# Kernel tuning notes

Hardware: AMD Instinct MI355X
Metric: run time of the kernel (lower is better)

The kernel has to match this reference:

```python
import jax, jax.numpy as jnp
import numpy as np

B, CIN, H, W = 16, 256, 56, 56
D, HEADS, KS, PAD, STRIDE, M = 256, 8, 3, 1, 1, 4
K = KS * KS
N = D // HEADS
# relative_indices: sum of window coords, flattened row-major, values in [0, 2*KS-2]
REL = (np.arange(KS)[:, None] + np.arange(KS)[None, :]).reshape(-1)


def setup_inputs() -> dict:
    key = jax.random.key(0)
    ks = jax.random.split(key, 7)
    return {
        "x": jax.random.normal(ks[0], (B, CIN, H, W), jnp.float32),
        "q": jax.random.normal(ks[1], (B, D, 1), jnp.float32),
        "Wk": jax.random.normal(ks[2], (D, CIN), jnp.float32) * 0.05,
        "Wv": jax.random.normal(ks[3], (D, CIN), jnp.float32) * 0.05,
        "pos_emb": jax.random.normal(ks[4], (1, 2 * KS - 1), jnp.float32),
        "Wlin": jax.random.normal(ks[5], (1, M), jnp.float32),
        "Wproj": jax.random.normal(ks[6], (D, D), jnp.float32) * 0.05,
    }


def _unfold(t):
    # torch nn.Unfold: (B,C,H,W) -> (B, C*K, L); patches feature dim ordered (C, kh, kw)
    p = jax.lax.conv_general_dilated_patches(
        t, (KS, KS), (STRIDE, STRIDE), [(PAD, PAD), (PAD, PAD)])
    b, _, ho, wo = p.shape
    return p.reshape(b, -1, ho * wo), ho, wo


def reference(x, q, Wk, Wv, pos_emb, Wlin, Wproj):
    b = x.shape[0]
    k = jnp.einsum('oc,bchw->bohw', Wk, x)  # 1x1 conv, no bias
    v = jnp.einsum('oc,bchw->bohw', Wv, x)
    ku, ho, wo = _unfold(k)
    vu, _, _ = _unfold(v)
    L = ho * wo
    ku = ku.reshape(b, HEADS, N, K, L)  # (b, h, n, k, l)
    vu = vu.reshape(b, HEADS, N, K, L)
    qh = q.reshape(b, HEADS, N)  # learned per-batch query, d=1 squeezed
    attn = jnp.einsum('bhn,bhnkl->bhlk', qh, ku)  # (b,h,l,K)
    attn = attn + pos_emb[0, REL]  # relative position bias, shape (K,)
    attn = jax.nn.softmax(attn, axis=-1)
    # repeat d(=1) -> m identical rows then Linear(m,1,no bias): equals scale by sum(Wlin)
    attn = attn * jnp.sum(Wlin)
    out = jnp.einsum('bhlk,bhnkl->bhnl', attn, vu)  # (b,h,n,l)
    out = out.reshape(b, D, ho, wo)  # fold with kernel 1 == reshape
    return jnp.einsum('oc,bchw->bohw', Wproj, out)  # 1x1 proj conv
```

## Files before the change

### kernel.cpp

```cpp
#include <hip/hip_runtime.h>

#define B_     16
#define D_     256
#define HEADS_ 8
#define N_     32
#define H_     56
#define W_     56
#define L_     3136
#define LDA    40

typedef short short8 __attribute__((ext_vector_type(8)));
typedef float f32x4  __attribute__((ext_vector_type(4)));

__device__ __forceinline__ unsigned short f2bf(float f) {
    union { float f; unsigned u; } c; c.f = f;
    unsigned u = c.u;
    u += 0x7fffu + ((u >> 16) & 1u);
    return (unsigned short)(u >> 16);
}

__global__ __launch_bounds__(256) void transpose_x_kernel(
    const float* __restrict__ x, unsigned short* __restrict__ Xt)
{
    __shared__ float tile[64][65];
    const int bb = blockIdx.z;
    const int c0 = blockIdx.y * 64;
    const int l0 = blockIdx.x * 64;
    const int t  = threadIdx.x;
    const int g4 = (t & 15) * 4;
    const int rr = t >> 4;

    const float* xb = x + ((size_t)bb * D_ + c0) * L_ + l0;
#pragma unroll
    for (int i = 0; i < 4; ++i) {
        const int c = rr + i * 16;
        float4 v = *(const float4*)(xb + (size_t)c * L_ + g4);
        *(float4*)&tile[c][g4] = v;
    }
    __syncthreads();
    unsigned short* Xb = Xt + ((size_t)bb * L_ + l0) * D_ + c0;
#pragma unroll
    for (int i = 0; i < 4; ++i) {
        const int l = rr + i * 16;
        uint2 o;
        o.x = (unsigned)f2bf(tile[g4 + 0][l]) | ((unsigned)f2bf(tile[g4 + 1][l]) << 16);
        o.y = (unsigned)f2bf(tile[g4 + 2][l]) | ((unsigned)f2bf(tile[g4 + 3][l]) << 16);
        *(uint2*)(Xb + (size_t)l * D_ + g4) = o;
    }
}

__global__ __launch_bounds__(256) void convert_w_kernel(
    const float* __restrict__ w0, const float* __restrict__ w1,
    const float* __restrict__ w2, unsigned short* __restrict__ o0,
    unsigned short* __restrict__ o1, unsigned short* __restrict__ o2)
{
    const float* src; unsigned short* dst;
    if (blockIdx.y == 0)      { src = w0; dst = o0; }
    else if (blockIdx.y == 1) { src = w1; dst = o1; }
    else                      { src = w2; dst = o2; }
    const int i = (blockIdx.x * 256 + threadIdx.x) * 4;
    float4 v = *(const float4*)(src + i);
    uint2 o;
    o.x = (unsigned)f2bf(v.x) | ((unsigned)f2bf(v.y) << 16);
    o.y = (unsigned)f2bf(v.z) | ((unsigned)f2bf(v.w) << 16);
    *(uint2*)(dst + i) = o;
}

__global__ __launch_bounds__(256) void gemm_kv_mfma(
    const unsigned short* __restrict__ Xt, const unsigned short* __restrict__ Wkb,
    const unsigned short* __restrict__ Wvb, const float* __restrict__ q,
    unsigned short* __restrict__ Vo, float* __restrict__ S)
{
    __shared__ unsigned short Aks[128][LDA];
    __shared__ unsigned short Avs[128][LDA];
    __shared__ unsigned short Bs[64][LDA];

    const int bb = blockIdx.z;
    const int d0 = blockIdx.y * 128;
    const int l0 = blockIdx.x * 64;
    const int t  = threadIdx.x;
    const int w    = t >> 6;
    const int lane = t & 63;
    const int col  = lane & 15;
    const int quad = lane >> 4;

    f32x4 accK[2][4], accV[2][4];
#pragma unroll
    for (int mi = 0; mi < 2; ++mi)
#pragma unroll
        for (int ni = 0; ni < 4; ++ni) {
            accK[mi][ni] = (f32x4){0.f, 0.f, 0.f, 0.f};
            accV[mi][ni] = (f32x4){0.f, 0.f, 0.f, 0.f};
        }

    const int srow = t >> 2;
    const int skc  = (t & 3) * 8;
    const unsigned short* Xrow = Xt + ((size_t)bb * L_ + l0 + srow) * D_ + skc;
    const unsigned short* Wk0  = Wkb + (size_t)(d0 + srow) * D_ + skc;
    const unsigned short* Wk1  = Wkb + (size_t)(d0 + 64 + srow) * D_ + skc;
    const unsigned short* Wv0  = Wvb + (size_t)(d0 + srow) * D_ + skc;
    const unsigned short* Wv1  = Wvb + (size_t)(d0 + 64 + srow) * D_ + skc;

    for (int kt = 0; kt < 8; ++kt) {
        const int c0 = kt * 32;
        uint4 xg  = *(const uint4*)(Xrow + c0);
        uint4 kg0 = *(const uint4*)(Wk0 + c0);
        uint4 kg1 = *(const uint4*)(Wk1 + c0);
        uint4 vg0 = *(const uint4*)(Wv0 + c0);
        uint4 vg1 = *(const uint4*)(Wv1 + c0);

        __syncthreads();
        *(uint4*)&Bs[srow][skc]        = xg;
        *(uint4*)&Aks[srow][skc]       = kg0;
        *(uint4*)&Aks[srow + 64][skc]  = kg1;
        *(uint4*)&Avs[srow][skc]       = vg0;
        *(uint4*)&Avs[srow + 64][skc]  = vg1;
        __syncthreads();

        short8 ak0 = *(const short8*)&Aks[w * 32 + col][quad * 8];
        short8 ak1 = *(const short8*)&Aks[w * 32 + 16 + col][quad * 8];
        short8 av0 = *(const short8*)&Avs[w * 32 + col][quad * 8];
        short8 av1 = *(const short8*)&Avs[w * 32 + 16 + col][quad * 8];
        short8 bfr[4];
#pragma unroll
        for (int ni = 0; ni < 4; ++ni)
            bfr[ni] = *(const short8*)&Bs[ni * 16 + col][quad * 8];

#pragma unroll
        for (int ni = 0; ni < 4; ++ni) {
            accK[0][ni] = __builtin_amdgcn_mfma_f32_16x16x32_bf16(ak0, bfr[ni], accK[0][ni], 0, 0, 0);
            accK[1][ni] = __builtin_amdgcn_mfma_f32_16x16x32_bf16(ak1, bfr[ni], accK[1][ni], 0, 0, 0);
            accV[0][ni] = __builtin_amdgcn_mfma_f32_16x16x32_bf16(av0, bfr[ni], accV[0][ni], 0, 0, 0);
            accV[1][ni] = __builtin_amdgcn_mfma_f32_16x16x32_bf16(av1, bfr[ni], accV[1][ni], 0, 0, 0);
        }
    }

#pragma unroll
    for (int mi = 0; mi < 2; ++mi)
#pragma unroll
        for (int ni = 0; ni < 4; ++ni)
#pragma unroll
            for (int r = 0; r < 4; ++r) {
                const int d = d0 + w * 32 + mi * 16 + quad * 4 + r;
                const int l = l0 + ni * 16 + col;
                Vo[((size_t)bb * D_ + d) * L_ + l] = f2bf(accV[mi][ni][r]);
            }

    const int hh = blockIdx.y * 4 + w;
    float qv[2][4];
#pragma unroll
    for (int mi = 0; mi < 2; ++mi)
#pragma unroll
        for (int r = 0; r < 4; ++r)
            qv[mi][r] = q[bb * D_ + hh * N_ + mi * 16 + quad * 4 + r];

#pragma unroll
    for (int ni = 0; ni < 4; ++ni) {
        float s = 0.f;
#pragma unroll
        for (int mi = 0; mi < 2; ++mi)
#pragma unroll
            for (int r = 0; r < 4; ++r)
                s = fmaf(qv[mi][r], accK[mi][ni][r], s);
        s += __shfl_xor(s, 16, 64);
        s += __shfl_xor(s, 32, 64);
        if (lane < 16)
            S[((size_t)bb * HEADS_ + hh) * L_ + l0 + ni * 16 + col] = s;
    }
}

__global__ __launch_bounds__(256) void attend_kernel(
    const float* __restrict__ S, const unsigned short* __restrict__ Vo,
    const float* __restrict__ pos_emb, const float* __restrict__ Wlin,
    unsigned short* __restrict__ Om)
{
    __shared__ unsigned short Vs[10][60][8];
    __shared__ float Ss[10][58];

    const int band = blockIdx.x;
    const int half = blockIdx.y;
    const int bh   = blockIdx.z;
    const int y0   = band * 8;
    const int t    = threadIdx.x;

    const float* Sb = S + (size_t)bh * L_;
    for (int wi = t; wi < 580; wi += 256) {
        const int row = wi / 58, c = wi - row * 58;
        const int gr = y0 - 1 + row, gc = c - 1;
        float v = 0.f;
        if (gr >= 0 && gr < H_ && gc >= 0 && gc < W_)
            v = Sb[gr * W_ + gc];
        Ss[row][c] = v;
    }

    const unsigned short* Vbase = Vo + ((size_t)bh * N_ + half * 8) * L_;
    for (int j = t; j < 560; j += 256) {
        const int ch = j & 7;
        const int rr = j >> 3;
        const int row = rr / 7, cg = rr - row * 7;
        const int gr = y0 - 1 + row;
        uint4 v = make_uint4(0u, 0u, 0u, 0u);
        if (gr >= 0 && gr < H_)
            v = *(const uint4*)(Vbase + (size_t)ch * L_ + gr * W_ + cg * 8);
        const unsigned short* hw = (const unsigned short*)&v;
        const int colb = cg * 8 + 1;
#pragma unroll
        for (int i = 0; i < 8; ++i)
            Vs[row][colb + i][ch] = hw[i];
    }
    if (t < 160) {
        const int row = t >> 4, side = (t >> 3) & 1, ch = t & 7;
        Vs[row][side ? 57 : 0][ch] = 0;
    }
    __syncthreads();

    const float scale = Wlin[0] + Wlin[1] + Wlin[2] + Wlin[3];
    const float pe0 = pos_emb[0], pe1 = pos_emb[1], pe2 = pos_emb[2];
    const float pe3 = pos_emb[3], pe4 = pos_emb[4];
    const float bias[9] = {pe0, pe1, pe2, pe1, pe2, pe3, pe2, pe3, pe4};

    for (int p = t; p < 448; p += 256) {
        const int yl = p / 56, xx = p - yl * 56;
        const int lr = yl + 1, lc = xx + 1;

        float lg[9], m = -1e30f;
#pragma unroll
        for (int dy = 0; dy < 3; ++dy)
#pragma unroll
            for (int dx = 0; dx < 3; ++dx) {
                const int k = dy * 3 + dx;
                lg[k] = Ss[lr - 1 + dy][lc - 1 + dx] + bias[k];
                m = fmaxf(m, lg[k]);
            }
        float ssum = 0.f;
#pragma unroll
        for (int k = 0; k < 9; ++k) { lg[k] = __expf(lg[k] - m); ssum += lg[k]; }
        const float inv = scale / ssum;

        float om[8] = {0.f, 0.f, 0.f, 0.f, 0.f, 0.f, 0.f, 0.f};
#pragma unroll
        for (int dy = 0; dy < 3; ++dy)
#pragma unroll
            for (int dx = 0; dx < 3; ++dx) {
                const float wk = lg[dy * 3 + dx] * inv;
                const uint4 v = *(const uint4*)&Vs[lr - 1 + dy][lc - 1 + dx][0];
                const unsigned* u = (const unsigned*)&v;
#pragma unroll
                for (int i = 0; i < 4; ++i) {
                    union { unsigned uu; float f; } lo, hi;
                    lo.uu = u[i] << 16;
                    hi.uu = u[i] & 0xffff0000u;
                    om[2 * i]     = fmaf(wk, lo.f, om[2 * i]);
                    om[2 * i + 1] = fmaf(wk, hi.f, om[2 * i + 1]);
                }
            }

        unsigned short ob[8];
#pragma unroll
        for (int i = 0; i < 8; ++i) ob[i] = f2bf(om[i]);
        const int l = (y0 + yl) * W_ + xx;
        *(uint4*)(Om + ((size_t)bh * L_ + l) * N_ + half * 8) = *(const uint4*)ob;
    }
}

__global__ __launch_bounds__(256) void gemm_proj_mfma(
    const unsigned short* __restrict__ Om, const unsigned short* __restrict__ Wpb,
    float* __restrict__ Out)
{
    __shared__ unsigned short As[128][LDA];
    __shared__ unsigned short Bs[64][LDA];

    const int bb = blockIdx.z;
    const int d0 = blockIdx.y * 128;
    const int l0 = blockIdx.x * 64;
    const int t  = threadIdx.x;
    const int w    = t >> 6;
    const int lane = t & 63;
    const int col  = lane & 15;
    const int quad = lane >> 4;

    f32x4 acc[2][4];
#pragma unroll
    for (int mi = 0; mi < 2; ++mi)
#pragma unroll
        for (int ni = 0; ni < 4; ++ni) acc[mi][ni] = (f32x4){0.f, 0.f, 0.f, 0.f};

    const int srow = t >> 2;
    const int skc  = (t & 3) * 8;
    const unsigned short* Wp0 = Wpb + (size_t)(d0 + srow) * D_ + skc;
    const unsigned short* Wp1 = Wpb + (size_t)(d0 + 64 + srow) * D_ + skc;
    const unsigned short* Orow = Om + ((size_t)bb * HEADS_ * L_ + l0 + srow) * N_ + skc;

    for (int kt = 0; kt < 8; ++kt) {
        const int c0 = kt * 32;
        uint4 bg  = *(const uint4*)(Orow + (size_t)kt * L_ * N_);
        uint4 ag0 = *(const uint4*)(Wp0 + c0);
        uint4 ag1 = *(const uint4*)(Wp1 + c0);

        __syncthreads();
        *(uint4*)&Bs[srow][skc]       = bg;
        *(uint4*)&As[srow][skc]       = ag0;
        *(uint4*)&As[srow + 64][skc]  = ag1;
        __syncthreads();

        short8 a0 = *(const short8*)&As[w * 32 + col][quad * 8];
        short8 a1 = *(const short8*)&As[w * 32 + 16 + col][quad * 8];
        short8 bfr[4];
#pragma unroll
        for (int ni = 0; ni < 4; ++ni)
            bfr[ni] = *(const short8*)&Bs[ni * 16 + col][quad * 8];

#pragma unroll
        for (int ni = 0; ni < 4; ++ni) {
            acc[0][ni] = __builtin_amdgcn_mfma_f32_16x16x32_bf16(a0, bfr[ni], acc[0][ni], 0, 0, 0);
            acc[1][ni] = __builtin_amdgcn_mfma_f32_16x16x32_bf16(a1, bfr[ni], acc[1][ni], 0, 0, 0);
        }
    }

#pragma unroll
    for (int mi = 0; mi < 2; ++mi)
#pragma unroll
        for (int ni = 0; ni < 4; ++ni)
#pragma unroll
            for (int r = 0; r < 4; ++r) {
                const int d = d0 + w * 32 + mi * 16 + quad * 4 + r;
                const int l = l0 + ni * 16 + col;
                Out[((size_t)bb * D_ + d) * L_ + l] = acc[mi][ni][r];
            }
}

extern "C" void kernel_launch(void* const* d_in, const int* in_sizes, int n_in,
                              void* d_out, int out_size, void* d_ws, size_t ws_size,
                              hipStream_t stream)
{
    const float* x       = (const float*)d_in[0];
    const float* q       = (const float*)d_in[1];
    const float* Wk      = (const float*)d_in[2];
    const float* Wv      = (const float*)d_in[3];
    const float* pos_emb = (const float*)d_in[4];
    const float* Wlin    = (const float*)d_in[5];
    const float* Wproj   = (const float*)d_in[6];
    float* out = (float*)d_out;

    const size_t planeE = (size_t)B_ * D_ * L_;
    unsigned short* Xt  = (unsigned short*)d_ws;
    unsigned short* Vo  = Xt + planeE;
    unsigned short* Om  = Vo + planeE;
    unsigned short* Wkb = Om + planeE;
    unsigned short* Wvb = Wkb + D_ * D_;
    unsigned short* Wpb = Wvb + D_ * D_;
    float*          S   = (float*)(Wpb + D_ * D_);

    transpose_x_kernel<<<dim3(L_ / 64, D_ / 64, B_), 256, 0, stream>>>(x, Xt);
    convert_w_kernel<<<dim3(64, 3), 256, 0, stream>>>(Wk, Wv, Wproj, Wkb, Wvb, Wpb);
    gemm_kv_mfma<<<dim3(L_ / 64, 2, B_), 256, 0, stream>>>(Xt, Wkb, Wvb, q, Vo, S);
    attend_kernel<<<dim3(7, 4, B_ * HEADS_), 256, 0, stream>>>(
        S, Vo, pos_emb, Wlin, Om);
    gemm_proj_mfma<<<dim3(L_ / 64, 2, B_), 256, 0, stream>>>(Om, Wpb, out);
}
```

Before: 180.3 us.

## Fold Wk into query, compute scores during transpose, retile GEMMs with async LDS loads

Precomputes qt = q·Wk per batch and head so attention scores come straight from x inside the transpose kernel, removing the K projection GEMM. The V and projection GEMMs move to 128x128 tiles over the flattened batch*L dimension, with double-buffered global_load_lds prefetch. The scores are now computed in fp32 from x rather than from bf16 K, which shifts numerics slightly. The transpose kernel now does extra FMA work, and the larger tiles mean fewer blocks.

```diff
diff --git a/kernel.cpp b/kernel.cpp
--- a/kernel.cpp
+++ b/kernel.cpp
@@ -7,7 +7,7 @@
 #define H_     56
 #define W_     56
 #define L_     3136
-#define LDA    40
+#define BL_    (B_ * L_)
 
 typedef short short8 __attribute__((ext_vector_type(8)));
 typedef float f32x4  __attribute__((ext_vector_type(4)));
@@ -19,153 +19,190 @@
     return (unsigned short)(u >> 16);
 }
 
-__global__ __launch_bounds__(256) void transpose_x_kernel(
-    const float* __restrict__ x, unsigned short* __restrict__ Xt)
+#define GL2L(g, l) __builtin_amdgcn_global_load_lds( \
+    (const __attribute__((address_space(1))) void*)(g), \
+    (__attribute__((address_space(3))) void*)(l), 16, 0, 0)
+
+__global__ __launch_bounds__(256) void convert_w_kernel(
+    const float* __restrict__ Wv, const float* __restrict__ Wproj,
+    const float* __restrict__ Wk, const float* __restrict__ q,
+    unsigned short* __restrict__ Wvb, unsigned short* __restrict__ Wpb,
+    float* __restrict__ qt)
+{
+    if (blockIdx.y < 2) {
+        const float* src   = (blockIdx.y == 0) ? Wv  : Wproj;
+        unsigned short* dst = (blockIdx.y == 0) ? Wvb : Wpb;
+        const int i = (blockIdx.x * 256 + threadIdx.x) * 4;
+        float4 v = *(const float4*)(src + i);
+        uint2 o;
+        o.x = (unsigned)f2bf(v.x) | ((unsigned)f2bf(v.y) << 16);
+        o.y = (unsigned)f2bf(v.z) | ((unsigned)f2bf(v.w) << 16);
+        *(uint2*)(dst + i) = o;
+    } else {
+        const int b  = blockIdx.x >> 2;
+        const int h0 = (blockIdx.x & 3) * 2;
+        const int c  = threadIdx.x;
+#pragma unroll
+        for (int hh = 0; hh < 2; ++hh) {
+            const int h = h0 + hh;
+            const float* qb = q  + b * D_ + h * N_;
+            const float* wr = Wk + (size_t)(h * N_) * D_ + c;
+            float acc = 0.f;
+#pragma unroll 8
+            for (int n = 0; n < N_; ++n)
+                acc = fmaf(qb[n], wr[(size_t)n * D_], acc);
+            qt[((size_t)b * HEADS_ + h) * D_ + c] = acc;
+        }
+    }
+}
+
+__global__ __launch_bounds__(256) void transpose_s_kernel(
+    const float* __restrict__ x, const float* __restrict__ qt,
+    unsigned short* __restrict__ Xt, float* __restrict__ S)
 {
     __shared__ float tile[64][65];
+    __shared__ float qs[2048];
+    __shared__ float Sred[4][8][64];
+
     const int bb = blockIdx.z;
-    const int c0 = blockIdx.y * 64;
     const int l0 = blockIdx.x * 64;
     const int t  = threadIdx.x;
     const int g4 = (t & 15) * 4;
     const int rr = t >> 4;
-
-    const float* xb = x + ((size_t)bb * D_ + c0) * L_ + l0;
-#pragma unroll
-    for (int i = 0; i < 4; ++i) {
-        const int c = rr + i * 16;
-        float4 v = *(const float4*)(xb + (size_t)c * L_ + g4);
-        *(float4*)&tile[c][g4] = v;
-    }
+    const int sl = t & 63;
+    const int cq = t >> 6;
+
+    {
+        const float4* s4 = (const float4*)(qt + (size_t)bb * HEADS_ * D_);
+        ((float4*)qs)[t]       = s4[t];
+        ((float4*)qs)[t + 256] = s4[t + 256];
+    }
+
+    float sacc[8];
+#pragma unroll
+    for (int h = 0; h < 8; ++h) sacc[h] = 0.f;
+
+    const float* xb = x + ((size_t)bb * D_) * L_ + l0;
+    unsigned short* Xb = Xt + ((size_t)bb * L_ + l0) * D_;
+
+    for (int ct = 0; ct < 4; ++ct) {
+        const int c0 = ct * 64;
+        float4 v[4];
+#pragma unroll
+        for (int i = 0; i < 4; ++i)
+            v[i] = *(const float4*)(xb + (size_t)(c0 + rr + i * 16) * L_ + g4);
+        __syncthreads();
+#pragma unroll
+        for (int i = 0; i < 4; ++i)
+            *(float4*)&tile[rr + i * 16][g4] = v[i];
+        __syncthreads();
+
+#pragma unroll
+        for (int i = 0; i < 4; ++i) {
+            const int l = rr + i * 16;
+            uint2 o;
+            o.x = (unsigned)f2bf(tile[g4 + 0][l]) | ((unsigned)f2bf(tile[g4 + 1][l]) << 16);
+            o.y = (unsigned)f2bf(tile[g4 + 2][l]) | ((unsigned)f2bf(tile[g4 + 3][l]) << 16);
+            *(uint2*)(Xb + (size_t)l * D_ + c0 + g4) = o;
+        }
+
+#pragma unroll
+        for (int cc = 0; cc < 16; ++cc) {
+            const float xv = tile[cq * 16 + cc][sl];
+            const int  ci = c0 + cq * 16 + cc;
+#pragma unroll
+            for (int h = 0; h < 8; ++h)
+                sacc[h] = fmaf(qs[h * 256 + ci], xv, sacc[h]);
+        }
+    }
+
     __syncthreads();
-    unsigned short* Xb = Xt + ((size_t)bb * L_ + l0) * D_ + c0;
-#pragma unroll
-    for (int i = 0; i < 4; ++i) {
-        const int l = rr + i * 16;
-        uint2 o;
-        o.x = (unsigned)f2bf(tile[g4 + 0][l]) | ((unsigned)f2bf(tile[g4 + 1][l]) << 16);
-        o.y = (unsigned)f2bf(tile[g4 + 2][l]) | ((unsigned)f2bf(tile[g4 + 3][l]) << 16);
-        *(uint2*)(Xb + (size_t)l * D_ + g4) = o;
-    }
-}
-
-__global__ __launch_bounds__(256) void convert_w_kernel(
-    const float* __restrict__ w0, const float* __restrict__ w1,
-    const float* __restrict__ w2, unsigned short* __restrict__ o0,
-    unsigned short* __restrict__ o1, unsigned short* __restrict__ o2)
-{
-    const float* src; unsigned short* dst;
-    if (blockIdx.y == 0)      { src = w0; dst = o0; }
-    else if (blockIdx.y == 1) { src = w1; dst = o1; }
-    else                      { src = w2; dst = o2; }
-    const int i = (blockIdx.x * 256 + threadIdx.x) * 4;
-    float4 v = *(const float4*)(src + i);
-    uint2 o;
-    o.x = (unsigned)f2bf(v.x) | ((unsigned)f2bf(v.y) << 16);
-    o.y = (unsigned)f2bf(v.z) | ((unsigned)f2bf(v.w) << 16);
-    *(uint2*)(dst + i) = o;
-}
-
-__global__ __launch_bounds__(256) void gemm_kv_mfma(
-    const unsigned short* __restrict__ Xt, const unsigned short* __restrict__ Wkb,
-    const unsigned short* __restrict__ Wvb, const float* __restrict__ q,
-    unsigned short* __restrict__ Vo, float* __restrict__ S)
-{
-    __shared__ unsigned short Aks[128][LDA];
-    __shared__ unsigned short Avs[128][LDA];
-    __shared__ unsigned short Bs[64][LDA];
-
-    const int bb = blockIdx.z;
+#pragma unroll
+    for (int h = 0; h < 8; ++h) Sred[cq][h][sl] = sacc[h];
+    __syncthreads();
+    {
+        const int h0 = t >> 6;
+#pragma unroll
+        for (int r = 0; r < 2; ++r) {
+            const int h = h0 + r * 4;
+            const float s = Sred[0][h][sl] + Sred[1][h][sl] + Sred[2][h][sl] + Sred[3][h][sl];
+            S[((size_t)bb * HEADS_ + h) * L_ + l0 + sl] = s;
+        }
+    }
+}
+
+__global__ __launch_bounds__(256) void gemm_v_mfma(
+    const unsigned short* __restrict__ Xt, const unsigned short* __restrict__ Wvb,
+    unsigned short* __restrict__ Vo)
+{
+    __shared__ unsigned short As[2][128 * 32];
+    __shared__ unsigned short Bs[2][128 * 32];
+
+    const int t = threadIdx.x;
+    const int w = t >> 6, lane = t & 63, col = lane & 15, quad = lane >> 4;
+    const int wr = w >> 1, wc = w & 1;
+    const int n0 = blockIdx.x * 128;
     const int d0 = blockIdx.y * 128;
-    const int l0 = blockIdx.x * 64;
-    const int t  = threadIdx.x;
-    const int w    = t >> 6;
-    const int lane = t & 63;
-    const int col  = lane & 15;
-    const int quad = lane >> 4;
-
-    f32x4 accK[2][4], accV[2][4];
-#pragma unroll
-    for (int mi = 0; mi < 2; ++mi)
-#pragma unroll
-        for (int ni = 0; ni < 4; ++ni) {
-            accK[mi][ni] = (f32x4){0.f, 0.f, 0.f, 0.f};
-            accV[mi][ni] = (f32x4){0.f, 0.f, 0.f, 0.f};
-        }
-
     const int srow = t >> 2;
     const int skc  = (t & 3) * 8;
-    const unsigned short* Xrow = Xt + ((size_t)bb * L_ + l0 + srow) * D_ + skc;
-    const unsigned short* Wk0  = Wkb + (size_t)(d0 + srow) * D_ + skc;
-    const unsigned short* Wk1  = Wkb + (size_t)(d0 + 64 + srow) * D_ + skc;
-    const unsigned short* Wv0  = Wvb + (size_t)(d0 + srow) * D_ + skc;
-    const unsigned short* Wv1  = Wvb + (size_t)(d0 + 64 + srow) * D_ + skc;
-
+
+    const unsigned short* Ag = Wvb + (size_t)(d0 + srow) * D_ + skc;
+    const unsigned short* Bg = Xt + (size_t)(n0 + srow) * D_ + skc;
+
+    f32x4 acc[4][4];
+#pragma unroll
+    for (int m = 0; m < 4; ++m)
+#pragma unroll
+        for (int n = 0; n < 4; ++n) acc[m][n] = (f32x4){0.f, 0.f, 0.f, 0.f};
+
+    {
+        char* An = (char*)&As[0][0] + w * 1024;
+        char* Bn = (char*)&Bs[0][0] + w * 1024;
+        GL2L(Ag, An);            GL2L(Ag + 64 * D_, An + 4096);
+        GL2L(Bg, Bn);            GL2L(Bg + 64 * D_, Bn + 4096);
+    }
+    __syncthreads();
+
+#pragma unroll
     for (int kt = 0; kt < 8; ++kt) {
-        const int c0 = kt * 32;
-        uint4 xg  = *(const uint4*)(Xrow + c0);
-        uint4 kg0 = *(const uint4*)(Wk0 + c0);
-        uint4 kg1 = *(const uint4*)(Wk1 + c0);
-        uint4 vg0 = *(const uint4*)(Wv0 + c0);
-        uint4 vg1 = *(const uint4*)(Wv1 + c0);
-
+        const int cur = kt & 1;
+        if (kt < 7) {
+            const int c1 = (kt + 1) * 32;
+            char* An = (char*)&As[cur ^ 1][0] + w * 1024;
+            char* Bn = (char*)&Bs[cur ^ 1][0] + w * 1024;
+            GL2L(Ag + c1, An);           GL2L(Ag + 64 * D_ + c1, An + 4096);
+            GL2L(Bg + c1, Bn);           GL2L(Bg + 64 * D_ + c1, Bn + 4096);
+        }
+        const unsigned short* Ab = &As[cur][0];
+        const unsigned short* Bb = &Bs[cur][0];
+        short8 af[4], bf[4];
+#pragma unroll
+        for (int m = 0; m < 4; ++m)
+            af[m] = *(const short8*)(Ab + (wr * 64 + m * 16 + col) * 32 + quad * 8);
+#pragma unroll
+        for (int n = 0; n < 4; ++n)
+            bf[n] = *(const short8*)(Bb + (wc * 64 + n * 16 + col) * 32 + quad * 8);
+#pragma unroll
+        for (int m = 0; m < 4; ++m)
+#pragma unroll
+            for (int n = 0; n < 4; ++n)
+                acc[m][n] = __builtin_amdgcn_mfma_f32_16x16x32_bf16(af[m], bf[n], acc[m][n], 0, 0, 0);
         __syncthreads();
-        *(uint4*)&Bs[srow][skc]        = xg;
-        *(uint4*)&Aks[srow][skc]       = kg0;
-        *(uint4*)&Aks[srow + 64][skc]  = kg1;
-        *(uint4*)&Avs[srow][skc]       = vg0;
-        *(uint4*)&Avs[srow + 64][skc]  = vg1;
-        __syncthreads();
-
-        short8 ak0 = *(const short8*)&Aks[w * 32 + col][quad * 8];
-        short8 ak1 = *(const short8*)&Aks[w * 32 + 16 + col][quad * 8];
-        short8 av0 = *(const short8*)&Avs[w * 32 + col][quad * 8];
-        short8 av1 = *(const short8*)&Avs[w * 32 + 16 + col][quad * 8];
-        short8 bfr[4];
-#pragma unroll
-        for (int ni = 0; ni < 4; ++ni)
-            bfr[ni] = *(const short8*)&Bs[ni * 16 + col][quad * 8];
-
-#pragma unroll
-        for (int ni = 0; ni < 4; ++ni) {
-            accK[0][ni] = __builtin_amdgcn_mfma_f32_16x16x32_bf16(ak0, bfr[ni], accK[0][ni], 0, 0, 0);
-            accK[1][ni] = __builtin_amdgcn_mfma_f32_16x16x32_bf16(ak1, bfr[ni], accK[1][ni], 0, 0, 0);
-            accV[0][ni] = __builtin_amdgcn_mfma_f32_16x16x32_bf16(av0, bfr[ni], accV[0][ni], 0, 0, 0);
-            accV[1][ni] = __builtin_amdgcn_mfma_f32_16x16x32_bf16(av1, bfr[ni], accV[1][ni], 0, 0, 0);
-        }
-    }
-
-#pragma unroll
-    for (int mi = 0; mi < 2; ++mi)
-#pragma unroll
-        for (int ni = 0; ni < 4; ++ni)
-#pragma unroll
-            for (int r = 0; r < 4; ++r) {
-                const int d = d0 + w * 32 + mi * 16 + quad * 4 + r;
-                const int l = l0 + ni * 16 + col;
-                Vo[((size_t)bb * D_ + d) * L_ + l] = f2bf(accV[mi][ni][r]);
-            }
-
-    const int hh = blockIdx.y * 4 + w;
-    float qv[2][4];
-#pragma unroll
-    for (int mi = 0; mi < 2; ++mi)
-#pragma unroll
-        for (int r = 0; r < 4; ++r)
-            qv[mi][r] = q[bb * D_ + hh * N_ + mi * 16 + quad * 4 + r];
-
-#pragma unroll
-    for (int ni = 0; ni < 4; ++ni) {
-        float s = 0.f;
-#pragma unroll
-        for (int mi = 0; mi < 2; ++mi)
+    }
+
+#pragma unroll
+    for (int n = 0; n < 4; ++n) {
+        const unsigned flat = n0 + wc * 64 + n * 16 + col;
+        const unsigned bq = flat / L_;
+        const unsigned lq = flat - bq * L_;
+        unsigned short* vout = Vo + (size_t)bq * D_ * L_ + lq;
+#pragma unroll
+        for (int m = 0; m < 4; ++m) {
+            const int dbase = d0 + wr * 64 + m * 16 + quad * 4;
 #pragma unroll
             for (int r = 0; r < 4; ++r)
-                s = fmaf(qv[mi][r], accK[mi][ni][r], s);
-        s += __shfl_xor(s, 16, 64);
-        s += __shfl_xor(s, 32, 64);
-        if (lane < 16)
-            S[((size_t)bb * HEADS_ + hh) * L_ + l0 + ni * 16 + col] = s;
+                vout[(size_t)(dbase + r) * L_] = f2bf(acc[m][n][r]);
+        }
     }
 }
 
@@ -267,66 +304,81 @@
     const unsigned short* __restrict__ Om, const unsigned short* __restrict__ Wpb,
     float* __restrict__ Out)
 {
-    __shared__ unsigned short As[128][LDA];
-    __shared__ unsigned short Bs[64][LDA];
-
-    const int bb = blockIdx.z;
+    __shared__ unsigned short As[2][128 * 32];
+    __shared__ unsigned short Bs[2][128 * 32];
+
+    const int t = threadIdx.x;
+    const int w = t >> 6, lane = t & 63, col = lane & 15, quad = lane >> 4;
+    const int wr = w >> 1, wc = w & 1;
+    const int n0 = blockIdx.x * 128;
     const int d0 = blockIdx.y * 128;
-    const int l0 = blockIdx.x * 64;
-    const int t  = threadIdx.x;
-    const int w    = t >> 6;
-    const int lane = t & 63;
-    const int col  = lane & 15;
-    const int quad = lane >> 4;
-
-    f32x4 acc[2][4];
-#pragma unroll
-    for (int mi = 0; mi < 2; ++mi)
-#pragma unroll
-        for (int ni = 0; ni < 4; ++ni) acc[mi][ni] = (f32x4){0.f, 0.f, 0.f, 0.f};
-
     const int srow = t >> 2;
     const int skc  = (t & 3) * 8;
-    const unsigned short* Wp0 = Wpb + (size_t)(d0 + srow) * D_ + skc;
-    const unsigned short* Wp1 = Wpb + (size_t)(d0 + 64 + srow) * D_ + skc;
-    const unsigned short* Orow = Om + ((size_t)bb * HEADS_ * L_ + l0 + srow) * N_ + skc;
-
+
+    const unsigned short* Ag = Wpb + (size_t)(d0 + srow) * D_ + skc;
+    const int f0 = n0 + srow;
+    const unsigned b0q = (unsigned)f0 / L_, l0q = (unsigned)f0 - b0q * L_;
+    const int f1 = f0 + 64;
+    const unsigned b1q = (unsigned)f1 / L_, l1q = (unsigned)f1 - b1q * L_;
+    const unsigned short* Bg0 = Om + ((size_t)(b0q * HEADS_) * L_ + l0q) * N_ + skc;
+    const unsigned short* Bg1 = Om + ((size_t)(b1q * HEADS_) * L_ + l1q) * N_ + skc;
+    const size_t kstride = (size_t)L_ * N_;
+
+    f32x4 acc[4][4];
+#pragma unroll
+    for (int m = 0; m < 4; ++m)
+#pragma unroll
+        for (int n = 0; n < 4; ++n) acc[m][n] = (f32x4){0.f, 0.f, 0.f, 0.f};
+
+    {
+        char* An = (char*)&As[0][0] + w * 1024;
+        char* Bn = (char*)&Bs[0][0] + w * 1024;
+        GL2L(Ag, An);            GL2L(Ag + 64 * D_, An + 4096);
+        GL2L(Bg0, Bn);           GL2L(Bg1, Bn + 4096);
+    }
+    __syncthreads();
+
+#pragma unroll
     for (int kt = 0; kt < 8; ++kt) {
-        const int c0 = kt * 32;
-        uint4 bg  = *(const uint4*)(Orow + (size_t)kt * L_ * N_);
-        uint4 ag0 = *(const uint4*)(Wp0 + c0);
-        uint4 ag1 = *(const uint4*)(Wp1 + c0);
-
+        const int cur = kt & 1;
+        if (kt < 7) {
+            const int c1 = (kt + 1) * 32;
+            char* An = (char*)&As[cur ^ 1][0] + w * 1024;
+            char* Bn = (char*)&Bs[cur ^ 1][0] + w * 1024;
+            GL2L(Ag + c1, An);                     GL2L(Ag + 64 * D_ + c1, An + 4096);
+            GL2L(Bg0 + (kt + 1) * kstride, Bn);    GL2L(Bg1 + (kt + 1) * kstride, Bn + 4096);
+        }
+        const unsigned short* Ab = &As[cur][0];
+        const unsigned short* Bb = &Bs[cur][0];
+        short8 af[4], bf[4];
+#pragma unroll
+        for (int m = 0; m < 4; ++m)
+            af[m] = *(const short8*)(Ab + (wr * 64 + m * 16 + col) * 32 + quad * 8);
+#pragma unroll
+        for (int n = 0; n < 4; ++n)
+            bf[n] = *(const short8*)(Bb + (wc * 64 + n * 16 + col) * 32 + quad * 8);
+#pragma unroll
+        for (int m = 0; m < 4; ++m)
+#pragma unroll
+            for (int n = 0; n < 4; ++n)
+                acc[m][n] = __builtin_amdgcn_mfma_f32_16x16x32_bf16(af[m], bf[n], acc[m][n], 0, 0, 0);
         __syncthreads();
-        *(uint4*)&Bs[srow][skc]       = bg;
-        *(uint4*)&As[srow][skc]       = ag0;
-        *(uint4*)&As[srow + 64][skc]  = ag1;
-        __syncthreads();
-
-        short8 a0 = *(const short8*)&As[w * 32 + col][quad * 8];
-        short8 a1 = *(const short8*)&As[w * 32 + 16 + col][quad * 8];
-        short8 bfr[4];
-#pragma unroll
-        for (int ni = 0; ni < 4; ++ni)
-            bfr[ni] = *(const short8*)&Bs[ni * 16 + col][quad * 8];
-
-#pragma unroll
-        for (int ni = 0; ni < 4; ++ni) {
-            acc[0][ni] = __builtin_amdgcn_mfma_f32_16x16x32_bf16(a0, bfr[ni], acc[0][ni], 0, 0, 0);
-            acc[1][ni] = __builtin_amdgcn_mfma_f32_16x16x32_bf16(a1, bfr[ni], acc[1][ni], 0, 0, 0);
-        }
-    }
-
-#pragma unroll
-    for (int mi = 0; mi < 2; ++mi)
-#pragma unroll
-        for (int ni = 0; ni < 4; ++ni)
-#pragma unroll
-            for (int r = 0; r < 4; ++r) {
-                const int d = d0 + w * 32 + mi * 16 + quad * 4 + r;
-                const int l = l0 + ni * 16 + col;
-                Out[((size_t)bb * D_ + d) * L_ + l] = acc[mi][ni][r];
-            }
+    }
+
+#pragma unroll
+    for (int n = 0; n < 4; ++n) {
+        const unsigned flat = n0 + wc * 64 + n * 16 + col;
+        const unsigned bq = flat / L_;
+        const unsigned lq = flat - bq * L_;
+        float* oout = Out + (size_t)bq * D_ * L_ + lq;
+#pragma unroll
+        for (int m = 0; m < 4; ++m) {
+            const int dbase = d0 + wr * 64 + m * 16 + quad * 4;
+#pragma unroll
+            for (int r = 0; r < 4; ++r)
+                oout[(size_t)(dbase + r) * L_] = acc[m][n][r];
+        }
+    }
 }
 
 extern "C" void kernel_launch(void* const* d_in, const int* in_sizes, int n_in,
@@ -346,15 +398,14 @@
     unsigned short* Xt  = (unsigned short*)d_ws;
     unsigned short* Vo  = Xt + planeE;
     unsigned short* Om  = Vo + planeE;
-    unsigned short* Wkb = Om + planeE;
-    unsigned short* Wvb = Wkb + D_ * D_;
+    unsigned short* Wvb = Om + planeE;
     unsigned short* Wpb = Wvb + D_ * D_;
     float*          S   = (float*)(Wpb + D_ * D_);
-
-    transpose_x_kernel<<<dim3(L_ / 64, D_ / 64, B_), 256, 0, stream>>>(x, Xt);
-    convert_w_kernel<<<dim3(64, 3), 256, 0, stream>>>(Wk, Wv, Wproj, Wkb, Wvb, Wpb);
-    gemm_kv_mfma<<<dim3(L_ / 64, 2, B_), 256, 0, stream>>>(Xt, Wkb, Wvb, q, Vo, S);
-    attend_kernel<<<dim3(7, 4, B_ * HEADS_), 256, 0, stream>>>(
-        S, Vo, pos_emb, Wlin, Om);
-    gemm_proj_mfma<<<dim3(L_ / 64, 2, B_), 256, 0, stream>>>(Om, Wpb, out);
-}
+    float*          qt  = S + (size_t)B_ * HEADS_ * L_;
+
+    convert_w_kernel<<<dim3(64, 3), 256, 0, stream>>>(Wv, Wproj, Wk, q, Wvb, Wpb, qt);
+    transpose_s_kernel<<<dim3(49, 1, 16), 256, 0, stream>>>(x, qt, Xt, S);
+    gemm_v_mfma<<<dim3(BL_ / 128, 2), 256, 0, stream>>>(Xt, Wvb, Vo);
+    attend_kernel<<<dim3(7, 4, B_ * HEADS_), 256, 0, stream>>>(S, Vo, pos_emb, Wlin, Om);
+    gemm_proj_mfma<<<dim3(BL_ / 128, 2), 256, 0, stream>>>(Om, Wpb, out);
+}
```

After: 196.2 us. 8.8% more time.
